# Performance work log

Measured on AMD Instinct MI355X. Metric: run time of the kernel, lower is better.

The kernel has to match this reference:

```python
import jax, jax.numpy as jnp
import numpy as np

N_NODES = 20000
N_EDGES = 320000
N_GRAPHS = 32
IN_CH = 5
HID = 64
HEADS = 4
DH = HID // HEADS  # 16
LAYERS = 8
EPS = 1e-5
SLOPE = 0.2


def setup_inputs() -> dict:
    key = jax.random.key(0)
    ks = jax.random.split(key, 32)
    inp = {}
    inp['x1'] = jax.random.normal(ks[0], (N_NODES, IN_CH), dtype=jnp.float32)
    inp['x2'] = jax.random.normal(ks[1], (N_NODES, IN_CH), dtype=jnp.float32)
    inp['edge_index1'] = jax.random.randint(ks[2], (2, N_EDGES), 0, N_NODES, dtype=jnp.int32)
    inp['edge_index2'] = jax.random.randint(ks[3], (2, N_EDGES), 0, N_NODES, dtype=jnp.int32)
    inp['batch1'] = jnp.sort(jax.random.randint(ks[4], (N_NODES,), 0, N_GRAPHS, dtype=jnp.int32))
    inp['batch2'] = jnp.sort(jax.random.randint(ks[5], (N_NODES,), 0, N_GRAPHS, dtype=jnp.int32))
    # node_lin
    inp['Wn'] = jax.random.normal(ks[6], (IN_CH, HID), dtype=jnp.float32) / np.sqrt(IN_CH)
    inp['bnode'] = jnp.zeros((HID,), dtype=jnp.float32)
    # GATv2 layers (stacked over LAYERS)
    s = 1.0 / np.sqrt(HID)
    inp['Wl'] = jax.random.normal(ks[7], (LAYERS, HID, HID), dtype=jnp.float32) * s
    inp['bl'] = jnp.zeros((LAYERS, HID), dtype=jnp.float32)
    inp['Wr'] = jax.random.normal(ks[8], (LAYERS, HID, HID), dtype=jnp.float32) * s
    inp['br'] = jnp.zeros((LAYERS, HID), dtype=jnp.float32)
    inp['att'] = jax.random.normal(ks[9], (LAYERS, HEADS, DH), dtype=jnp.float32) / np.sqrt(DH)
    inp['cbias'] = jnp.zeros((LAYERS, HID), dtype=jnp.float32)
    # batch norms
    inp['gamma'] = jnp.ones((LAYERS, HID), dtype=jnp.float32)
    inp['beta'] = jnp.zeros((LAYERS, HID), dtype=jnp.float32)
    # fc head
    inp['f1w'] = jax.random.normal(ks[10], (2 * HID, 256), dtype=jnp.float32) / np.sqrt(2 * HID)
    inp['f1b'] = jnp.zeros((256,), dtype=jnp.float32)
    inp['f2w'] = jax.random.normal(ks[11], (256, 128), dtype=jnp.float32) / np.sqrt(256)
    inp['f2b'] = jnp.zeros((128,), dtype=jnp.float32)
    inp['f3w'] = jax.random.normal(ks[12], (128, 1), dtype=jnp.float32) / np.sqrt(128)
    inp['f3b'] = jnp.zeros((1,), dtype=jnp.float32)
    return inp


def _gatv2_layer(x, src, dst, Wl, bl, Wr, br, att, bias):
    # x: [N, HID]; src/dst: [E'] (self loops included)
    N = x.shape[0]
    xl = (x @ Wl + bl).reshape(N, HEADS, DH)  # source transform
    xr = (x @ Wr + br).reshape(N, HEADS, DH)  # target transform
    e = jax.nn.leaky_relu(xl[src] + xr[dst], SLOPE)          # [E, H, DH]
    score = jnp.einsum('ehd,hd->eh', e, att)                  # [E, H]
    smax = jax.ops.segment_max(score, dst, num_segments=N)    # [N, H]
    ex = jnp.exp(score - smax[dst])
    denom = jax.ops.segment_sum(ex, dst, num_segments=N)
    alpha = ex / denom[dst]                                   # [E, H]
    msg = alpha[:, :, None] * xl[src]                         # [E, H, DH]
    out = jax.ops.segment_sum(msg, dst, num_segments=N)       # [N, H, DH]
    return out.reshape(N, HID) + bias


def _forward_once(x, edge_index, batch, Wn, bnode, Wl, bl, Wr, br, att, cbias, gamma, beta):
    N = x.shape[0]
    loop = jnp.arange(N, dtype=edge_index.dtype)
    src = jnp.concatenate([edge_index[0], loop])  # add_self_loops=True
    dst = jnp.concatenate([edge_index[1], loop])
    h = x @ Wn + bnode
    for l in range(LAYERS):
        g = _gatv2_layer(h, src, dst, Wl[l], bl[l], Wr[l], br[l], att[l], cbias[l])
        mu = g.mean(axis=0)
        var = g.var(axis=0)
        g = (g - mu) / jnp.sqrt(var + EPS) * gamma[l] + beta[l]
        h = h + jax.nn.elu(g)
    # global_mean_pool
    sums = jax.ops.segment_sum(h, batch, num_segments=N_GRAPHS)
    cnt = jax.ops.segment_sum(jnp.ones((N,), dtype=h.dtype), batch, num_segments=N_GRAPHS)
    return sums / jnp.maximum(cnt, 1.0)[:, None]


def reference(x1, edge_index1, batch1, x2, edge_index2, batch2, Wn, bnode, Wl, bl, Wr, br, att, cbias, gamma, beta, f1w, f1b, f2w, f2b, f3w, f3b):
    o1 = _forward_once(x1, edge_index1, batch1, Wn, bnode, Wl, bl, Wr, br, att, cbias, gamma, beta)
    o2 = _forward_once(x2, edge_index2, batch2, Wn, bnode, Wl, bl, Wr, br, att, cbias, gamma, beta)
    c = jnp.concatenate([o1, o2], axis=1)           # [G, 128]
    h = jax.nn.relu(c @ f1w + f1b)                   # dropout = identity (eval)
    h = jax.nn.relu(h @ f2w + f2b)
    return h @ f3w + f3b                             # [G, 1]
```

## Files before the change

### kernel.cpp

```cpp
#include <hip/hip_runtime.h>
#include <hip/hip_bf16.h>
#include <hip/hip_fp16.h>

#define N_NODES 20000
#define HID 64
#define EPS 1e-5f

struct GP {
    const int* ei;
    const int* batch;
    const float* x;
    int* deg;
    int* cursor;
    int* csr;
    float* h;
    __half* xlh;
    float* xr;
    float* gb;
    float* stats;
    float* osum;
};


__global__ void k_csr_init(GP a, GP b, int n, int two) {
    int t = blockIdx.x * blockDim.x + threadIdx.x;
    if (t < n) {
        a.deg[t] = 1;
        if (two) b.deg[t] = 1;
    }
}

__global__ void k_count(GP a, GP b, int Ea, int Eb, int two) {
    int t = blockIdx.x * blockDim.x + threadIdx.x;
    if (t < Ea) atomicAdd(&a.deg[a.ei[Ea + t]], 1);
    if (two && t < Eb) atomicAdd(&b.deg[b.ei[Eb + t]], 1);
}

#define SCAN_T 1024
#define SCAN_C 20
__global__ __launch_bounds__(1024) void k_scan(GP a, GP b, int n, int totA, int totB) {
    GP g = blockIdx.x ? b : a;
    int total = blockIdx.x ? totB : totA;
    __shared__ int sd[SCAN_T];
    int t = threadIdx.x;
    int base = t * SCAN_C;
    int loc[SCAN_C];
    int s = 0;
#pragma unroll
    for (int i = 0; i < SCAN_C; ++i) {
        int idx = base + i;
        loc[i] = (idx < n) ? g.deg[idx] : 0;
        s += loc[i];
    }
    sd[t] = s;
    __syncthreads();
    for (int off = 1; off < SCAN_T; off <<= 1) {
        int v = (t >= off) ? sd[t - off] : 0;
        __syncthreads();
        sd[t] += v;
        __syncthreads();
    }
    int run = sd[t] - s;
#pragma unroll
    for (int i = 0; i < SCAN_C; ++i) {
        int idx = base + i;
        if (idx < n) { g.deg[idx] = run; g.cursor[idx] = run; run += loc[i]; }
    }
    if (t == 0) g.deg[n] = total;
}

__global__ void k_scatter(GP a, GP b, int Ea, int Eb, int n, int two) {
    int t = blockIdx.x * blockDim.x + threadIdx.x;
    if (t < Ea) {
        int s = a.ei[t], d = a.ei[Ea + t];
        a.csr[atomicAdd(&a.cursor[d], 1)] = s;
    } else if (t < Ea + n) {
        int nn = t - Ea;
        a.csr[atomicAdd(&a.cursor[nn], 1)] = nn;
    }
    if (two) {
        if (t < Eb) {
            int s = b.ei[t], d = b.ei[Eb + t];
            b.csr[atomicAdd(&b.cursor[d], 1)] = s;
        } else if (t < Eb + n) {
            int nn = t - Eb;
            b.csr[atomicAdd(&b.cursor[nn], 1)] = nn;
        }
    }
}


__global__ void k_nodelin(GP a, GP b, int nPer, const float* __restrict__ Wn,
                          const float* __restrict__ bn, int n) {
    int bid = blockIdx.x;
    GP g = a;
    if (bid >= nPer) { g = b; bid -= nPer; }
    int idx = bid * 256 + threadIdx.x;
    if (idx >= n * HID) return;
    int node = idx >> 6, c = idx & 63;
    float acc = bn[c];
#pragma unroll
    for (int k = 0; k < 5; ++k) acc += g.x[node * 5 + k] * Wn[k * HID + c];
    g.h[idx] = acc;
}


__global__ __launch_bounds__(256) void k_lin2(GP ga, GP gbp, int nPer, int n,
        const float* __restrict__ Wl, const float* __restrict__ bl,
        const float* __restrict__ Wr, const float* __restrict__ br,
        const float* __restrict__ gamma, const float* __restrict__ beta, int layer) {
    __shared__ float wls[4096], wrs[4096];
    __shared__ float hs[2048];
    int bid = blockIdx.x;
    GP g = ga;
    if (bid >= nPer) { g = gbp; bid -= nPer; }
    {
        const float4* wl4 = (const float4*)Wl;
        const float4* wr4 = (const float4*)Wr;
        float4* l4 = (float4*)wls;
        float4* r4 = (float4*)wrs;
        for (int i = threadIdx.x; i < 1024; i += 256) { l4[i] = wl4[i]; r4[i] = wr4[i]; }
    }
    int c = threadIdx.x & 63;
    int wid = threadIdx.x >> 6;
    float blv = bl[c], brv = br[c];
    float mu = 0.f, inv = 1.f, gam = 1.f, bet = 0.f;
    if (layer > 0) {
        const float* st = g.stats + (layer - 1) * 128;
        float invn = 1.0f / (float)n;
        mu = st[c] * invn;
        float var = st[64 + c] * invn - mu * mu;
        inv = rsqrtf(fmaxf(var, 0.f) + EPS);
        gam = gamma[c]; bet = beta[c];
    }
    __syncthreads();
    float* hw = &hs[wid * 512];
    const float4* hw4 = (const float4*)hw;
    for (int base = bid * 32; base < n; base += nPer * 32) {
        int nb = base + wid * 8;
        size_t off0 = (size_t)nb * 64 + c;
        float hv[8];
        if (layer > 0) {
#pragma unroll
            for (int j = 0; j < 8; ++j) {
                float gv = g.gb[off0 + j * 64];
                float ov = g.h[off0 + j * 64];
                float v = (gv - mu) * inv * gam + bet;
                v = v > 0.f ? v : expm1f(v);
                hv[j] = ov + v;
                g.h[off0 + j * 64] = hv[j];
            }
        } else {
#pragma unroll
            for (int j = 0; j < 8; ++j) hv[j] = g.h[off0 + j * 64];
        }
#pragma unroll
        for (int j = 0; j < 8; ++j) hw[j * 64 + c] = hv[j];
        float accl[8], accr[8];
#pragma unroll
        for (int j = 0; j < 8; ++j) { accl[j] = blv; accr[j] = brv; }
        for (int k4 = 0; k4 < 16; ++k4) {
            float4 hq[8];
#pragma unroll
            for (int j = 0; j < 8; ++j) hq[j] = hw4[j * 16 + k4];
#pragma unroll
            for (int kk = 0; kk < 4; ++kk) {
                float wl = wls[(k4 * 4 + kk) * 64 + c];
                float wr = wrs[(k4 * 4 + kk) * 64 + c];
#pragma unroll
                for (int j = 0; j < 8; ++j) {
                    float hx = (&hq[j].x)[kk];
                    accl[j] = fmaf(hx, wl, accl[j]);
                    accr[j] = fmaf(hx, wr, accr[j]);
                }
            }
        }
#pragma unroll
        for (int j = 0; j < 8; ++j) {
            g.xlh[off0 + j * 64] = __float2half(accl[j]);
            g.xr[off0 + j * 64] = accr[j];
        }
    }
}


__device__ __forceinline__ float red16(float p) {
    p += __int_as_float(__builtin_amdgcn_update_dpp(0, __float_as_int(p), 0xB1, 0xF, 0xF, true));
    p += __int_as_float(__builtin_amdgcn_update_dpp(0, __float_as_int(p), 0x4E, 0xF, 0xF, true));
    p += __int_as_float(__builtin_amdgcn_update_dpp(0, __float_as_int(p), 0x141, 0xF, 0xF, true));
    p += __int_as_float(__builtin_amdgcn_update_dpp(0, __float_as_int(p), 0x140, 0xF, 0xF, true));
    return p;
}

__global__ __launch_bounds__(1024) void k_attn(GP ga, GP gbp, int nPer,
        const float* __restrict__ att, const float* __restrict__ cbias, int layer, int n) {
    int bid = blockIdx.x;
    GP g = (bid & 1) ? gbp : ga;
    bid >>= 1;
    int lane = threadIdx.x & 63;
    int wid = threadIdx.x >> 6;
    int gw = bid * 16 + wid;
    int nw = nPer * 16;
    float attv = att[lane];
    float attv2 = attv * 0.2f;
    float cb = cbias[lane];
    const int* __restrict__ rowptr = g.deg;
    const int* __restrict__ csr = g.csr;
    const __half* __restrict__ xl = g.xlh;
    const float* __restrict__ xr = g.xr;
    float* __restrict__ gbuf = g.gb;
    float* st = g.stats + layer * 128;
    float bsum = 0.f, bsq = 0.f;
    for (int node = gw; node < n; node += nw) {
        int start = rowptr[node], end = rowptr[node + 1];
        float xrv = xr[(size_t)node * 64 + lane];
        float xself = __half2float(xl[(size_t)node * 64 + lane]);
        float ts = xself + xrv;
        float sself = red16(ts * (ts > 0.f ? attv : attv2));
        float lsum = 0.f, acc = 0.f;
        int idx = start;
        for (; idx + 8 <= end; idx += 8) {
            int sidx[8];
            float xv[8];
#pragma unroll
            for (int j = 0; j < 8; ++j) sidx[j] = csr[idx + j];
#pragma unroll
            for (int j = 0; j < 8; ++j) xv[j] = __half2float(xl[(size_t)sidx[j] * 64 + lane]);
#pragma unroll
            for (int j = 0; j < 8; ++j) {
                float t = xv[j] + xrv;
                float p = red16(t * (t > 0.f ? attv : attv2));
                float w = __expf(fminf(p - sself, 80.f));
                lsum += w;
                acc = fmaf(w, xv[j], acc);
            }
        }
        for (; idx + 4 <= end; idx += 4) {
            int sidx[4];
            float xv[4];
#pragma unroll
            for (int j = 0; j < 4; ++j) sidx[j] = csr[idx + j];
#pragma unroll
            for (int j = 0; j < 4; ++j) xv[j] = __half2float(xl[(size_t)sidx[j] * 64 + lane]);
#pragma unroll
            for (int j = 0; j < 4; ++j) {
                float t = xv[j] + xrv;
                float p = red16(t * (t > 0.f ? attv : attv2));
                float w = __expf(fminf(p - sself, 80.f));
                lsum += w;
                acc = fmaf(w, xv[j], acc);
            }
        }
        for (; idx < end; ++idx) {
            int s0 = csr[idx];
            float x0 = __half2float(xl[(size_t)s0 * 64 + lane]);
            float t0 = x0 + xrv;
            float p0 = red16(t0 * (t0 > 0.f ? attv : attv2));
            float w0 = __expf(fminf(p0 - sself, 80.f));
            lsum += w0;
            acc = fmaf(w0, x0, acc);
        }
        float outv = acc / lsum + cb;
        gbuf[(size_t)node * 64 + lane] = outv;
        bsum += outv; bsq += outv * outv;
    }
    __shared__ float sred[1024];
    sred[threadIdx.x] = bsum;
    __syncthreads();
    if (threadIdx.x < 64) {
        float t = 0.f;
#pragma unroll
        for (int w = 0; w < 16; ++w) t += sred[w * 64 + threadIdx.x];
        atomicAdd(&st[threadIdx.x], t);
    }
    __syncthreads();
    sred[threadIdx.x] = bsq;
    __syncthreads();
    if (threadIdx.x < 64) {
        float t = 0.f;
#pragma unroll
        for (int w = 0; w < 16; ++w) t += sred[w * 64 + threadIdx.x];
        atomicAdd(&st[64 + threadIdx.x], t);
    }
}


__global__ __launch_bounds__(256) void k_pool(GP ga, GP gbp, int nPer,
        const float* __restrict__ gamma, const float* __restrict__ beta, int n) {
    int bid = blockIdx.x;
    GP g = ga;
    if (bid >= nPer) { g = gbp; bid -= nPer; }
    int lane = threadIdx.x & 63, w = threadIdx.x >> 6;
    const float* st = g.stats + 7 * 128;
    float invn = 1.f / (float)n;
    float mu = st[lane] * invn;
    float var = st[64 + lane] * invn - mu * mu;
    float inv = rsqrtf(fmaxf(var, 0.f) + EPS);
    float gam = gamma[lane], bet = beta[lane];
    int chunk = (n + nPer - 1) / nPer;
    int s = bid * chunk;
    int e = min(s + chunk, n);
    float acc = 0.f;
    int cur = -1;
    for (int node = s + w; node < e; node += 4) {
        int bg = g.batch[node];
        size_t off = (size_t)node * 64 + lane;
        float gv = g.gb[off];
        float hv = g.h[off];
        float v = (gv - mu) * inv * gam + bet;
        float hn = hv + (v > 0.f ? v : expm1f(v));
        if (bg != cur) {
            if (cur >= 0) atomicAdd(&g.osum[cur * 64 + lane], acc);
            acc = 0.f; cur = bg;
        }
        acc += hn;
    }
    if (cur >= 0) atomicAdd(&g.osum[cur * 64 + lane], acc);
}


__device__ __forceinline__ int lb(const int* __restrict__ b, int n, int v) {
    int lo = 0, hi = n;
    while (lo < hi) { int mid = (lo + hi) >> 1; if (b[mid] < v) lo = mid + 1; else hi = mid; }
    return lo;
}

__global__ __launch_bounds__(256) void k_fc(const float* __restrict__ o1, const float* __restrict__ o2,
                                            const int* __restrict__ b1, const int* __restrict__ b2,
                                            const float* __restrict__ f1w, const float* __restrict__ f1b,
                                            const float* __restrict__ f2w, const float* __restrict__ f2b,
                                            const float* __restrict__ f3w, const float* __restrict__ f3b,
                                            float* __restrict__ out, int n) {
    int gid = blockIdx.x, t = threadIdx.x;
    __shared__ float cin[128];
    __shared__ float h1[256];
    __shared__ float red[128];
    __shared__ int cnts[2];
    if (t == 0) cnts[0] = lb(b1, n, gid + 1) - lb(b1, n, gid);
    if (t == 1) cnts[1] = lb(b2, n, gid + 1) - lb(b2, n, gid);
    __syncthreads();
    if (t < 64) {
        float c1 = (float)(cnts[0] > 0 ? cnts[0] : 1);
        float c2 = (float)(cnts[1] > 0 ? cnts[1] : 1);
        cin[t] = o1[gid * 64 + t] / c1;
        cin[64 + t] = o2[gid * 64 + t] / c2;
    }
    __syncthreads();
    float a = f1b[t];
#pragma unroll 8
    for (int k = 0; k < 128; ++k) a += cin[k] * f1w[k * 256 + t];
    h1[t] = fmaxf(a, 0.f);
    __syncthreads();
    if (t < 128) {
        float a2 = f2b[t];
#pragma unroll 8
        for (int k = 0; k < 256; ++k) a2 += h1[k] * f2w[k * 128 + t];
        red[t] = fmaxf(a2, 0.f) * f3w[t];
    }
    __syncthreads();
    for (int off = 64; off > 0; off >>= 1) {
        if (t < off) red[t] += red[t + off];
        __syncthreads();
    }
    if (t == 0) out[gid] = red[0] + f3b[0];
}


extern "C" void kernel_launch(void* const* d_in, const int* in_sizes, int n_in,
                              void* d_out, int out_size, void* d_ws, size_t ws_size,
                              hipStream_t stream) {
    const float* x1 = (const float*)d_in[0];
    const float* x2 = (const float*)d_in[1];
    const int* ei1 = (const int*)d_in[2];
    const int* ei2 = (const int*)d_in[3];
    const int* b1 = (const int*)d_in[4];
    const int* b2 = (const int*)d_in[5];
    const float* Wn = (const float*)d_in[6];
    const float* bnode = (const float*)d_in[7];
    const float* Wl = (const float*)d_in[8];
    const float* bl = (const float*)d_in[9];
    const float* Wr = (const float*)d_in[10];
    const float* br = (const float*)d_in[11];
    const float* att = (const float*)d_in[12];
    const float* cbias = (const float*)d_in[13];
    const float* gamma = (const float*)d_in[14];
    const float* beta = (const float*)d_in[15];
    const float* f1w = (const float*)d_in[16];
    const float* f1b = (const float*)d_in[17];
    const float* f2w = (const float*)d_in[18];
    const float* f2b = (const float*)d_in[19];
    const float* f3w = (const float*)d_in[20];
    const float* f3b = (const float*)d_in[21];
    float* out = (float*)d_out;

    const int N = N_NODES;
    const int EA = in_sizes[2] / 2;
    const int EB = in_sizes[3] / 2;
    const size_t INT_PG = 20096 + 20096 + 340096;
    const size_t BIG = (size_t)N * 64;
    const size_t SMALL = 2 * 1024 + 2 * 2048;
    const size_t dualBytes = 2 * INT_PG * 4 + (8 * BIG + SMALL) * 4;
    const int dual = (ws_size >= dualBytes) ? 1 : 0;

    int* ibase = (int*)d_ws;
    int* iA = ibase;
    int* iB = dual ? ibase + INT_PG : ibase;
    float* fbase = (float*)(ibase + (size_t)(dual ? 2 : 1) * INT_PG);
    float* hA = fbase;
    float* xlA = hA + BIG;
    float* xrA = xlA + BIG;
    float* gbA = xrA + BIG;
    float* hB = dual ? gbA + BIG : hA;
    float* xlB = dual ? hB + BIG : xlA;
    float* xrB = dual ? xlB + BIG : xrA;
    float* gbB = dual ? xrB + BIG : gbA;
    float* small = dual ? gbB + BIG : gbA + BIG;
    float* statsA = small;
    float* statsB = small + 1024;
    float* osumA = small + 2048;
    float* osumB = small + 4096;

    GP A, B;
    A.ei = ei1; A.batch = b1; A.x = x1;
    A.deg = iA; A.cursor = iA + 20096; A.csr = iA + 40192;
    A.h = hA; A.xlh = (__half*)xlA; A.xr = xrA; A.gb = gbA; A.stats = statsA; A.osum = osumA;
    B.ei = ei2; B.batch = b2; B.x = x2;
    B.deg = iB; B.cursor = iB + 20096; B.csr = iB + 40192;
    B.h = hB; B.xlh = (__half*)xlB; B.xr = xrB; B.gb = gbB; B.stats = statsB; B.osum = osumB;

    hipMemsetAsync(small, 0, SMALL * sizeof(float), stream);

    const int LIN2_NB = 320;
    const int ATT_NB = 256;
    const int POOL_NB = 250;

    if (dual) {
        int Emax = EA > EB ? EA : EB;
        k_csr_init<<<(N + 255) / 256, 256, 0, stream>>>(A, B, N, 1);
        k_count<<<(Emax + 255) / 256, 256, 0, stream>>>(A, B, EA, EB, 1);
        k_scan<<<2, 1024, 0, stream>>>(A, B, N, EA + N, EB + N);
        k_scatter<<<(Emax + N + 255) / 256, 256, 0, stream>>>(A, B, EA, EB, N, 1);
        k_nodelin<<<2 * ((N * 64) / 256), 256, 0, stream>>>(A, B, (N * 64) / 256, Wn, bnode, N);
        for (int l = 0; l < 8; ++l) {
            const float* gm = l ? gamma + (l - 1) * 64 : gamma;
            const float* bt = l ? beta + (l - 1) * 64 : beta;
            k_lin2<<<2 * LIN2_NB, 256, 0, stream>>>(A, B, LIN2_NB, N, Wl + l * 4096, bl + l * 64,
                                                    Wr + l * 4096, br + l * 64, gm, bt, l);
            k_attn<<<2 * ATT_NB, 1024, 0, stream>>>(A, B, ATT_NB, att + l * 64, cbias + l * 64, l, N);
        }
        k_pool<<<2 * POOL_NB, 256, 0, stream>>>(A, B, POOL_NB, gamma + 7 * 64, beta + 7 * 64, N);
    } else {
        for (int gi = 0; gi < 2; ++gi) {
            GP G = gi ? B : A;
            int E = gi ? EB : EA;
            k_csr_init<<<(N + 255) / 256, 256, 0, stream>>>(G, G, N, 0);
            k_count<<<(E + 255) / 256, 256, 0, stream>>>(G, G, E, E, 0);
            k_scan<<<1, 1024, 0, stream>>>(G, G, N, E + N, E + N);
            k_scatter<<<(E + N + 255) / 256, 256, 0, stream>>>(G, G, E, E, N, 0);
            k_nodelin<<<(N * 64) / 256, 256, 0, stream>>>(G, G, (N * 64) / 256, Wn, bnode, N);
            for (int l = 0; l < 8; ++l) {
                const float* gm = l ? gamma + (l - 1) * 64 : gamma;
                const float* bt = l ? beta + (l - 1) * 64 : beta;
                k_lin2<<<LIN2_NB, 256, 0, stream>>>(G, G, LIN2_NB, N, Wl + l * 4096, bl + l * 64,
                                                    Wr + l * 4096, br + l * 64, gm, bt, l);
                k_attn<<<2 * ATT_NB, 1024, 0, stream>>>(G, G, ATT_NB, att + l * 64, cbias + l * 64, l, N);
            }
            k_pool<<<POOL_NB, 256, 0, stream>>>(G, G, POOL_NB, gamma + 7 * 64, beta + 7 * 64, N);
        }
    }
    k_fc<<<32, 256, 0, stream>>>(osumA, osumB, b1, b2, f1w, f1b, f2w, f2b, f3w, f3b, out, N);
}
```

Before: 693.5 us.

## Use MFMA fp16 for node linear layers and precompute byte offsets in CSR

The per-layer dual linear transform moves from scalar FP32 FMAs to 16x16x32 fp16 MFMA instructions. Weights are transposed into padded fp16 LDS tiles, and each block now covers one 64-node tile, with the grid sized to match. Separately, the CSR stores source indices pre-multiplied by the row byte stride, and attention folds log2(e) into the attention vector so it can use exp2f. The cost is lower precision, since the fp16 inputs now also feed the xr path, and the scatter output now carries byte offsets whose products could overflow for larger graphs.

```diff
diff --git a/kernel.cpp b/kernel.cpp
--- a/kernel.cpp
+++ b/kernel.cpp
@@ -5,6 +5,9 @@
 #define N_NODES 20000
 #define HID 64
 #define EPS 1e-5f
+
+typedef _Float16 half8 __attribute__((ext_vector_type(8)));
+typedef float f32x4 __attribute__((ext_vector_type(4)));
 
 struct GP {
     const int* ei;
@@ -73,18 +76,18 @@
     int t = blockIdx.x * blockDim.x + threadIdx.x;
     if (t < Ea) {
         int s = a.ei[t], d = a.ei[Ea + t];
-        a.csr[atomicAdd(&a.cursor[d], 1)] = s;
+        a.csr[atomicAdd(&a.cursor[d], 1)] = s * 128;
     } else if (t < Ea + n) {
         int nn = t - Ea;
-        a.csr[atomicAdd(&a.cursor[nn], 1)] = nn;
+        a.csr[atomicAdd(&a.cursor[nn], 1)] = nn * 128;
     }
     if (two) {
         if (t < Eb) {
             int s = b.ei[t], d = b.ei[Eb + t];
-            b.csr[atomicAdd(&b.cursor[d], 1)] = s;
+            b.csr[atomicAdd(&b.cursor[d], 1)] = s * 128;
         } else if (t < Eb + n) {
             int nn = t - Eb;
-            b.csr[atomicAdd(&b.cursor[nn], 1)] = nn;
+            b.csr[atomicAdd(&b.cursor[nn], 1)] = nn * 128;
         }
     }
 }
@@ -109,76 +112,75 @@
         const float* __restrict__ Wl, const float* __restrict__ bl,
         const float* __restrict__ Wr, const float* __restrict__ br,
         const float* __restrict__ gamma, const float* __restrict__ beta, int layer) {
-    __shared__ float wls[4096], wrs[4096];
-    __shared__ float hs[2048];
+    __shared__ _Float16 wT[128 * 72];
+    __shared__ _Float16 hT[64 * 72];
     int bid = blockIdx.x;
     GP g = ga;
     if (bid >= nPer) { g = gbp; bid -= nPer; }
+    int tid = threadIdx.x;
+    int lane = tid & 63;
+    int w = tid >> 6;
+    int quad = lane >> 4;
+    int m = lane & 15;
+
+    for (int i = tid; i < 4096; i += 256) {
+        int k = i >> 6, c = i & 63;
+        wT[c * 72 + k] = (_Float16)Wl[i];
+        wT[(c + 64) * 72 + k] = (_Float16)Wr[i];
+    }
+
+    int base = bid * 64;
     {
-        const float4* wl4 = (const float4*)Wl;
-        const float4* wr4 = (const float4*)Wr;
-        float4* l4 = (float4*)wls;
-        float4* r4 = (float4*)wrs;
-        for (int i = threadIdx.x; i < 1024; i += 256) { l4[i] = wl4[i]; r4[i] = wr4[i]; }
-    }
-    int c = threadIdx.x & 63;
-    int wid = threadIdx.x >> 6;
-    float blv = bl[c], brv = br[c];
-    float mu = 0.f, inv = 1.f, gam = 1.f, bet = 0.f;
-    if (layer > 0) {
-        const float* st = g.stats + (layer - 1) * 128;
-        float invn = 1.0f / (float)n;
-        mu = st[c] * invn;
-        float var = st[64 + c] * invn - mu * mu;
-        inv = rsqrtf(fmaxf(var, 0.f) + EPS);
-        gam = gamma[c]; bet = beta[c];
-    }
-    __syncthreads();
-    float* hw = &hs[wid * 512];
-    const float4* hw4 = (const float4*)hw;
-    for (int base = bid * 32; base < n; base += nPer * 32) {
-        int nb = base + wid * 8;
-        size_t off0 = (size_t)nb * 64 + c;
-        float hv[8];
+        float mu = 0.f, inv = 1.f, gam = 1.f, bet = 0.f;
         if (layer > 0) {
-#pragma unroll
-            for (int j = 0; j < 8; ++j) {
-                float gv = g.gb[off0 + j * 64];
-                float ov = g.h[off0 + j * 64];
-                float v = (gv - mu) * inv * gam + bet;
-                v = v > 0.f ? v : expm1f(v);
-                hv[j] = ov + v;
-                g.h[off0 + j * 64] = hv[j];
-            }
-        } else {
-#pragma unroll
-            for (int j = 0; j < 8; ++j) hv[j] = g.h[off0 + j * 64];
-        }
-#pragma unroll
-        for (int j = 0; j < 8; ++j) hw[j * 64 + c] = hv[j];
-        float accl[8], accr[8];
-#pragma unroll
-        for (int j = 0; j < 8; ++j) { accl[j] = blv; accr[j] = brv; }
-        for (int k4 = 0; k4 < 16; ++k4) {
-            float4 hq[8];
-#pragma unroll
-            for (int j = 0; j < 8; ++j) hq[j] = hw4[j * 16 + k4];
-#pragma unroll
-            for (int kk = 0; kk < 4; ++kk) {
-                float wl = wls[(k4 * 4 + kk) * 64 + c];
-                float wr = wrs[(k4 * 4 + kk) * 64 + c];
-#pragma unroll
-                for (int j = 0; j < 8; ++j) {
-                    float hx = (&hq[j].x)[kk];
-                    accl[j] = fmaf(hx, wl, accl[j]);
-                    accr[j] = fmaf(hx, wr, accr[j]);
+            const float* st = g.stats + (layer - 1) * 128;
+            float invn = 1.0f / (float)n;
+            mu = st[lane] * invn;
+            float var = st[64 + lane] * invn - mu * mu;
+            inv = rsqrtf(fmaxf(var, 0.f) + EPS);
+            gam = gamma[lane]; bet = beta[lane];
+        }
+#pragma unroll
+        for (int it = 0; it < 16; ++it) {
+            int rr = it * 4 + w;
+            int node = base + rr;
+            float hv = 0.f;
+            if (node < n) {
+                size_t off = (size_t)node * 64 + lane;
+                if (layer > 0) {
+                    float gv = g.gb[off];
+                    float ov = g.h[off];
+                    float v = (gv - mu) * inv * gam + bet;
+                    v = v > 0.f ? v : expm1f(v);
+                    hv = ov + v;
+                    g.h[off] = hv;
+                } else {
+                    hv = g.h[off];
                 }
             }
-        }
-#pragma unroll
-        for (int j = 0; j < 8; ++j) {
-            g.xlh[off0 + j * 64] = __float2half(accl[j]);
-            g.xr[off0 + j * 64] = accr[j];
+            hT[rr * 72 + lane] = (_Float16)hv;
+        }
+    }
+    __syncthreads();
+
+    half8 a0 = *(const half8*)&hT[(w * 16 + m) * 72 + quad * 8];
+    half8 a1 = *(const half8*)&hT[(w * 16 + m) * 72 + 32 + quad * 8];
+#pragma unroll
+    for (int cg = 0; cg < 8; ++cg) {
+        half8 b0 = *(const half8*)&wT[(cg * 16 + m) * 72 + quad * 8];
+        half8 b1 = *(const half8*)&wT[(cg * 16 + m) * 72 + 32 + quad * 8];
+        f32x4 acc = {0.f, 0.f, 0.f, 0.f};
+        acc = __builtin_amdgcn_mfma_f32_16x16x32_f16(a0, b0, acc, 0, 0, 0);
+        acc = __builtin_amdgcn_mfma_f32_16x16x32_f16(a1, b1, acc, 0, 0, 0);
+        float bias = (cg < 4) ? bl[cg * 16 + m] : br[(cg - 4) * 16 + m];
+#pragma unroll
+        for (int reg = 0; reg < 4; ++reg) {
+            int node = base + w * 16 + quad * 4 + reg;
+            if (node < n) {
+                float v = acc[reg] + bias;
+                if (cg < 4) g.xlh[(size_t)node * 64 + cg * 16 + m] = __float2half(v);
+                else        g.xr[(size_t)node * 64 + (cg - 4) * 16 + m] = v;
+            }
         }
     }
 }
@@ -201,12 +203,12 @@
     int wid = threadIdx.x >> 6;
     int gw = bid * 16 + wid;
     int nw = nPer * 16;
-    float attv = att[lane];
+    float attv = att[lane] * 1.44269504f;
     float attv2 = attv * 0.2f;
     float cb = cbias[lane];
     const int* __restrict__ rowptr = g.deg;
     const int* __restrict__ csr = g.csr;
-    const __half* __restrict__ xl = g.xlh;
+    const char* xlb = (const char*)g.xlh + (size_t)lane * 2;
     const float* __restrict__ xr = g.xr;
     float* __restrict__ gbuf = g.gb;
     float* st = g.stats + layer * 128;
@@ -214,49 +216,49 @@
     for (int node = gw; node < n; node += nw) {
         int start = rowptr[node], end = rowptr[node + 1];
         float xrv = xr[(size_t)node * 64 + lane];
-        float xself = __half2float(xl[(size_t)node * 64 + lane]);
+        float xself = __half2float(*(const __half*)(xlb + (size_t)node * 128));
         float ts = xself + xrv;
         float sself = red16(ts * (ts > 0.f ? attv : attv2));
         float lsum = 0.f, acc = 0.f;
         int idx = start;
         for (; idx + 8 <= end; idx += 8) {
-            int sidx[8];
+            int off[8];
             float xv[8];
 #pragma unroll
-            for (int j = 0; j < 8; ++j) sidx[j] = csr[idx + j];
-#pragma unroll
-            for (int j = 0; j < 8; ++j) xv[j] = __half2float(xl[(size_t)sidx[j] * 64 + lane]);
+            for (int j = 0; j < 8; ++j) off[j] = csr[idx + j];
+#pragma unroll
+            for (int j = 0; j < 8; ++j) xv[j] = __half2float(*(const __half*)(xlb + off[j]));
 #pragma unroll
             for (int j = 0; j < 8; ++j) {
                 float t = xv[j] + xrv;
                 float p = red16(t * (t > 0.f ? attv : attv2));
-                float w = __expf(fminf(p - sself, 80.f));
+                float w = exp2f(fminf(p - sself, 110.f));
                 lsum += w;
                 acc = fmaf(w, xv[j], acc);
             }
         }
         for (; idx + 4 <= end; idx += 4) {
-            int sidx[4];
+            int off[4];
             float xv[4];
 #pragma unroll
-            for (int j = 0; j < 4; ++j) sidx[j] = csr[idx + j];
-#pragma unroll
-            for (int j = 0; j < 4; ++j) xv[j] = __half2float(xl[(size_t)sidx[j] * 64 + lane]);
+            for (int j = 0; j < 4; ++j) off[j] = csr[idx + j];
+#pragma unroll
+            for (int j = 0; j < 4; ++j) xv[j] = __half2float(*(const __half*)(xlb + off[j]));
 #pragma unroll
             for (int j = 0; j < 4; ++j) {
                 float t = xv[j] + xrv;
                 float p = red16(t * (t > 0.f ? attv : attv2));
-                float w = __expf(fminf(p - sself, 80.f));
+                float w = exp2f(fminf(p - sself, 110.f));
                 lsum += w;
                 acc = fmaf(w, xv[j], acc);
             }
         }
         for (; idx < end; ++idx) {
-            int s0 = csr[idx];
-            float x0 = __half2float(xl[(size_t)s0 * 64 + lane]);
+            int o = csr[idx];
+            float x0 = __half2float(*(const __half*)(xlb + o));
             float t0 = x0 + xrv;
             float p0 = red16(t0 * (t0 > 0.f ? attv : attv2));
-            float w0 = __expf(fminf(p0 - sself, 80.f));
+            float w0 = exp2f(fminf(p0 - sself, 110.f));
             lsum += w0;
             acc = fmaf(w0, x0, acc);
         }
@@ -430,7 +432,7 @@
 
     hipMemsetAsync(small, 0, SMALL * sizeof(float), stream);
 
-    const int LIN2_NB = 320;
+    const int LIN2_NB = (N + 63) / 64;
     const int ATT_NB = 256;
     const int POOL_NB = 250;
 
```

Result: slower. 723.1 us (+4.3%).
